# Kernel optimization log

Hardware: AMD Instinct MI355X
Metric: run time of the kernel (lower is better)

The kernel has to match this reference:

```python
import jax, jax.numpy as jnp
import numpy as np

B, S, D, H = 2, 2048, 1024, 16


def setup_inputs() -> dict:
    key = jax.random.key(0)
    kq, kk, kv1, kv2 = jax.random.split(key, 4)
    return {
        "q": jax.random.normal(kq, (B, S, D), dtype=jnp.float32),
        "k": jax.random.normal(kk, (B, S, D), dtype=jnp.float32),
        "v1": jax.random.normal(kv1, (B, S, D), dtype=jnp.float32),
        "v2": jax.random.normal(kv2, (B, S, D), dtype=jnp.float32),
        "num_attn_heads": 16,
    }


def _split_heads(x, h):
    b, s, d = x.shape
    return x.reshape(b, s, h, d // h).transpose(0, 2, 1, 3)  # [B,H,S,dh]


def reference(q, k, v1, v2, num_attn_heads):
    h = num_attn_heads
    b, s, d = q.shape
    dh = d // h
    qh = _split_heads(q, h)
    kh = _split_heads(k, h)
    v1h = _split_heads(v1, h)
    v2h = _split_heads(v2, h)
    scores = jnp.einsum("bhqd,bhkd->bhqk", qh, kh) / jnp.sqrt(jnp.float32(dh))
    # Faithful to create_mask(input, 0): nopeek = triu(ones, k=0); mask = (nopeek == 0)
    # -> only STRICTLY lower triangle is visible; diagonal and above get -1e9.
    # Row 0 is fully masked -> softmax uniform (same as torch behavior).
    allowed = jnp.tril(jnp.ones((s, s), dtype=bool), k=-1)  # [S,S] j < i
    scores = jnp.where(allowed[None, None], scores, jnp.float32(-1e9))
    p_attn = jax.nn.softmax(scores, axis=-1)  # dropout p=0.0 -> identity
    o1 = jnp.einsum("bhqk,bhkd->bhqd", p_attn, v1h)
    o2 = jnp.einsum("bhqk,bhkd->bhqd", p_attn, v2h)
    o1 = o1.transpose(0, 2, 1, 3).reshape(b, s, d)
    o2 = o2.transpose(0, 2, 1, 3).reshape(b, s, d)
    return (o1, o2)
```

## Files before the change

### kernel.cpp

```cpp
#include <hip/hip_runtime.h>

#define B_ 2
#define S_ 2048
#define D_ 1024
#define H_ 16
#define DH 64
#define OFF2 (B_ * S_ * D_)
#define ELEMS (B_ * H_ * S_ * DH)

typedef __attribute__((ext_vector_type(8))) __bf16 bf16x8;
typedef __attribute__((ext_vector_type(4))) float f32x4;
typedef __attribute__((ext_vector_type(4))) unsigned int u32x4;
typedef __attribute__((ext_vector_type(2))) unsigned int u32x2;
typedef __attribute__((address_space(3))) unsigned int lds_u32;
typedef __attribute__((address_space(1))) const unsigned int glob_u32;

__device__ __forceinline__ unsigned short f2bf(float f) {
    return __builtin_bit_cast(unsigned short, (__bf16)f);
}
__device__ __forceinline__ unsigned int pk2(float a, float b) {
    return (unsigned int)f2bf(a) | ((unsigned int)f2bf(b) << 16);
}
__device__ __forceinline__ float bf2f(unsigned short h) {
    unsigned int u = ((unsigned int)h) << 16;
    return __builtin_bit_cast(float, u);
}

__global__ void prep_all(const float* __restrict__ k,
                         const float* __restrict__ v1, const float* __restrict__ v2,
                         unsigned short* __restrict__ kb,
                         unsigned short* __restrict__ v1t, unsigned short* __restrict__ v2t) {
    int id = blockIdx.x;
    if (id < 2048) {
        int cid = id * 256 + threadIdx.x;
        int d8 = cid & 7;
        int s  = (cid >> 3) & (S_ - 1);
        int h  = (cid >> 14) & (H_ - 1);
        int b  = cid >> 18;
        int off = (b * S_ + s) * D_ + h * DH + d8 * 8;
        float4 f0 = *(const float4*)(k + off);
        float4 f1 = *(const float4*)(k + off + 4);
        u32x4 wv = {pk2(f0.x, f0.y), pk2(f0.z, f0.w),
                    pk2(f1.x, f1.y), pk2(f1.z, f1.w)};
        *(u32x4*)(kb + cid * 8) = wv;
        return;
    }
    __shared__ __align__(16) unsigned short ldsT[64][72];
    int id2 = id - 2048;
    int t = threadIdx.x;
    int s0 = (id2 & 31) * 64;
    int bh = (id2 >> 5) & 31;
    int b = bh >> 4, h = bh & 15;
    const float* src = (id2 >> 10) ? v2 : v1;
    unsigned short* dst = (id2 >> 10) ? v2t : v1t;
    {
        int sl = t >> 2, dc = t & 3;
        int off = (b * S_ + s0 + sl) * D_ + h * DH + dc * 16;
#pragma unroll
        for (int i4 = 0; i4 < 4; i4++) {
            float4 f = *(const float4*)(src + off + i4 * 4);
            int d = dc * 16 + i4 * 4;
            ldsT[d + 0][sl] = f2bf(f.x);
            ldsT[d + 1][sl] = f2bf(f.y);
            ldsT[d + 2][sl] = f2bf(f.z);
            ldsT[d + 3][sl] = f2bf(f.w);
        }
    }
    __syncthreads();
    {
        int d = t >> 2, sc = t & 3;
        u32x4 a = *(const u32x4*)(&ldsT[d][sc * 16]);
        u32x4 c = *(const u32x4*)(&ldsT[d][sc * 16 + 8]);
        int off = (bh * DH + d) * S_ + s0 + sc * 16;
        *(u32x4*)(dst + off) = a;
        *(u32x4*)(dst + off + 8) = c;
    }
}

__global__ __launch_bounds__(256) void flash_attn(
        const float* __restrict__ qf, const unsigned short* __restrict__ kb,
        const unsigned short* __restrict__ v1t, const unsigned short* __restrict__ v2t,
        float* __restrict__ out) {
    __shared__ __align__(16) unsigned short sK0[4096], sK1[4096];
    __shared__ __align__(16) unsigned short sV1[4096], sV2[4096];

    int tid = threadIdx.x;
    int w = tid >> 6, lane = tid & 63;
    int lr = lane & 15, lg = lane >> 4;
    int srow = tid >> 3, sco = tid & 7;

    int id = blockIdx.x;
    int xcd = id & 7;
    int j = id >> 3;
    int bh = xcd * 4 + (j & 3);
    int qt = 31 - (j >> 2);
    int b = bh >> 4, hh = bh & 15;

    const unsigned short* gK  = kb  + bh * (S_ * DH);
    const unsigned short* gV1 = v1t + bh * (DH * S_);
    const unsigned short* gV2 = v2t + bh * (DH * S_);

    auto stageV = [&](int t) {
#pragma unroll
        for (int jj = 0; jj < 2; jj++) {
            int row = srow + jj * 32;
            int cosw = (sco ^ (row & 7)) * 8;
            int c8 = (tid + jj * 256) * 8;
            __builtin_amdgcn_global_load_lds((glob_u32*)(gV1 + row * S_ + t * 64 + cosw),
                                             (lds_u32*)(sV1 + c8), 16, 0, 0);
            __builtin_amdgcn_global_load_lds((glob_u32*)(gV2 + row * S_ + t * 64 + cosw),
                                             (lds_u32*)(sV2 + c8), 16, 0, 0);
        }
    };
    auto stageK = [&](unsigned short* dK, int t) {
#pragma unroll
        for (int jj = 0; jj < 2; jj++) {
            int row = srow + jj * 32;
            int cosw = (sco ^ (row & 7)) * 8;
            int c8 = (tid + jj * 256) * 8;
            __builtin_amdgcn_global_load_lds((glob_u32*)(gK + (t * 64 + row) * 64 + cosw),
                                             (lds_u32*)(dK + c8), 16, 0, 0);
        }
    };

    bf16x8 qa[2];
    {
        const float qs = 0.125f * 1.4426950408889634f;
        const float* a = qf + ((size_t)b * S_ + qt * 64 + w * 16 + lr) * D_ + hh * DH + lg * 8;
        float4 q0 = *(const float4*)a;
        float4 q1 = *(const float4*)(a + 4);
        float4 q2 = *(const float4*)(a + 32);
        float4 q3 = *(const float4*)(a + 36);
        u32x4 w0 = {pk2(q0.x * qs, q0.y * qs), pk2(q0.z * qs, q0.w * qs),
                    pk2(q1.x * qs, q1.y * qs), pk2(q1.z * qs, q1.w * qs)};
        u32x4 w1 = {pk2(q2.x * qs, q2.y * qs), pk2(q2.z * qs, q2.w * qs),
                    pk2(q3.x * qs, q3.y * qs), pk2(q3.z * qs, q3.w * qs)};
        qa[0] = __builtin_bit_cast(bf16x8, w0);
        qa[1] = __builtin_bit_cast(bf16x8, w1);
    }

    f32x4 acc1[4], acc2[4];
#pragma unroll
    for (int dt = 0; dt < 4; dt++) {
        acc1[dt] = (f32x4){0.f, 0.f, 0.f, 0.f};
        acc2[dt] = (f32x4){0.f, 0.f, 0.f, 0.f};
    }
    float l = 0.f;

    stageK(sK0, 0);

    for (int t = 0; t <= qt; t++) {
        const unsigned short* cK = (t & 1) ? sK1 : sK0;
        unsigned short* nK       = (t & 1) ? sK0 : sK1;
        __builtin_amdgcn_s_barrier();
        stageV(t);
        stageK(nK, (t < qt) ? t + 1 : qt);
        asm volatile("s_waitcnt vmcnt(6)" ::: "memory");
        f32x4 s[4];
        __builtin_amdgcn_s_setprio(1);
#pragma unroll
        for (int n = 0; n < 4; n++) {
            int kv = n * 16 + lr;
            int ix0 = ((kv << 6) + lg * 8) ^ ((kv & 7) << 3);
            int ix1 = ((kv << 6) + 32 + lg * 8) ^ ((kv & 7) << 3);
            bf16x8 k0 = __builtin_bit_cast(bf16x8, *(const u32x4*)(cK + ix0));
            bf16x8 k1 = __builtin_bit_cast(bf16x8, *(const u32x4*)(cK + ix1));
            f32x4 a = __builtin_amdgcn_mfma_f32_16x16x32_bf16(
                k0, qa[0], (f32x4){-20.f, -20.f, -20.f, -20.f}, 0, 0, 0);
            s[n] = __builtin_amdgcn_mfma_f32_16x16x32_bf16(k1, qa[1], a, 0, 0, 0);
        }
        __builtin_amdgcn_s_setprio(0);
        if (t == qt) {
#pragma unroll
            for (int n = 0; n < 4; n++)
#pragma unroll
                for (int r = 0; r < 4; r++)
                    if (n * 16 + lg * 4 + r >= w * 16 + lr) s[n][r] = -1e30f;
        }
        u32x4 pa[2];
#pragma unroll
        for (int ks = 0; ks < 2; ks++) {
            float p0[4], p1[4];
#pragma unroll
            for (int r = 0; r < 4; r++) {
                p0[r] = __builtin_amdgcn_exp2f(s[2 * ks][r] - 20.0f);
                p1[r] = __builtin_amdgcn_exp2f(s[2 * ks + 1][r] - 20.0f);
                l += p0[r] + p1[r];
            }
            unsigned int u0 = pk2(p0[0], p0[1]);
            unsigned int u1 = pk2(p0[2], p0[3]);
            unsigned int u2 = pk2(p1[0], p1[1]);
            unsigned int u3 = pk2(p1[2], p1[3]);
            u32x2 ab = __builtin_amdgcn_permlane32_swap(u0, u2, false, false);
            u32x2 cd = __builtin_amdgcn_permlane32_swap(u1, u3, false, false);
            u32x2 ab2 = __builtin_amdgcn_permlane16_swap(ab[0], ab[1], false, false);
            u32x2 cd2 = __builtin_amdgcn_permlane16_swap(cd[0], cd[1], false, false);
            pa[ks] = (u32x4){ab2[0], cd2[0], ab2[1], cd2[1]};
        }
        asm volatile("s_waitcnt vmcnt(2)" ::: "memory");
        __builtin_amdgcn_s_barrier();
        __builtin_amdgcn_s_setprio(1);
#pragma unroll
        for (int ks = 0; ks < 2; ks++) {
            bf16x8 pab = __builtin_bit_cast(bf16x8, pa[ks]);
#pragma unroll
            for (int dt = 0; dt < 4; dt++) {
                int d = dt * 16 + lr;
                int vix = ((d << 6) + ks * 32 + lg * 8) ^ ((d & 7) << 3);
                bf16x8 vf1 = __builtin_bit_cast(bf16x8, *(const u32x4*)(sV1 + vix));
                acc1[dt] = __builtin_amdgcn_mfma_f32_16x16x32_bf16(vf1, pab, acc1[dt], 0, 0, 0);
                bf16x8 vf2 = __builtin_bit_cast(bf16x8, *(const u32x4*)(sV2 + vix));
                acc2[dt] = __builtin_amdgcn_mfma_f32_16x16x32_bf16(vf2, pab, acc2[dt], 0, 0, 0);
            }
        }
        __builtin_amdgcn_s_setprio(0);
    }

    asm volatile("s_waitcnt vmcnt(0)" ::: "memory");

    float lt = l;
    lt += __shfl_xor(lt, 16, 64);
    lt += __shfl_xor(lt, 32, 64);
    float inv = 1.0f / lt;
    {
        int qrow = qt * 64 + w * 16 + lr;
        int base = (b * S_ + qrow) * D_ + hh * DH + lg * 4;
#pragma unroll
        for (int dt = 0; dt < 4; dt++) {
            f32x4 o1 = acc1[dt] * inv;
            f32x4 o2 = acc2[dt] * inv;
            *(f32x4*)(out + base + dt * 16) = o1;
            *(f32x4*)(out + base + dt * 16 + OFF2) = o2;
        }
    }
}

__global__ void row0_mean(const unsigned short* __restrict__ v1t,
                          const unsigned short* __restrict__ v2t,
                          float* __restrict__ out) {
    int wid = blockIdx.x * 4 + (threadIdx.x >> 6);
    int lane = threadIdx.x & 63;
    int tz = wid >> 11;
    int bhd = wid & 2047;
    const unsigned short* src = (tz ? v2t : v1t) + bhd * S_;
    float sum = 0.f;
#pragma unroll
    for (int kk = 0; kk < 4; kk++) {
        u32x4 v = *(const u32x4*)(src + (kk * 64 + lane) * 8);
#pragma unroll
        for (int jj = 0; jj < 4; jj++) {
            unsigned int u = v[jj];
            sum += bf2f((unsigned short)(u & 0xffff)) + bf2f((unsigned short)(u >> 16));
        }
    }
#pragma unroll
    for (int msk = 32; msk >= 1; msk >>= 1) sum += __shfl_xor(sum, msk, 64);
    if (lane == 0) {
        int b = bhd >> 10, rem = bhd & 1023, h = rem >> 6, d = rem & 63;
        out[tz * OFF2 + b * (S_ * D_) + h * DH + d] = sum * (1.0f / S_);
    }
}

extern "C" void kernel_launch(void* const* d_in, const int* in_sizes, int n_in,
                              void* d_out, int out_size, void* d_ws, size_t ws_size,
                              hipStream_t stream) {
    const float* q  = (const float*)d_in[0];
    const float* k  = (const float*)d_in[1];
    const float* v1 = (const float*)d_in[2];
    const float* v2 = (const float*)d_in[3];
    float* out = (float*)d_out;

    unsigned short* kb  = (unsigned short*)d_ws;
    unsigned short* v1t = kb + ELEMS;
    unsigned short* v2t = v1t + ELEMS;

    prep_all<<<4096, 256, 0, stream>>>(k, v1, v2, kb, v1t, v2t);
    flash_attn<<<1024, 256, 0, stream>>>(q, kb, v1t, v2t, out);
    row0_mean<<<1024, 256, 0, stream>>>(v1t, v2t, out);
}
```

Baseline: 66.69 us.

## Fold row-0 mean into attention kernel and prefetch first K/V tiles early

Removes the separate row0_mean launch by appending 1024 extra blocks to flash_attn that compute the uniform-softmax output for row 0. Attention blocks now skip writing row 0 so the two block types do not write the same output. The prologue now issues the Q loads and the first K, V and next-K tile transfers before the Q bf16 conversion, so memory latency overlaps setup, and the loop skips the barrier and staging on its first iteration. The redundant -20 subtraction before exp2 is dropped, since the MFMA accumulator init already applies that offset and the normalisation cancels it.

```diff
diff --git a/kernel.cpp b/kernel.cpp
--- a/kernel.cpp
+++ b/kernel.cpp
@@ -85,11 +85,37 @@
     __shared__ __align__(16) unsigned short sV1[4096], sV2[4096];
 
     int tid = threadIdx.x;
+    int id = blockIdx.x;
+
+    if (id >= 1024) {
+        int wid = (id - 1024) * 4 + (tid >> 6);
+        int lane = tid & 63;
+        int tz = wid >> 11;
+        int bhd = wid & 2047;
+        const unsigned short* src = (tz ? v2t : v1t) + bhd * S_;
+        float sum = 0.f;
+#pragma unroll
+        for (int kk = 0; kk < 4; kk++) {
+            u32x4 v = *(const u32x4*)(src + (kk * 64 + lane) * 8);
+#pragma unroll
+            for (int jj = 0; jj < 4; jj++) {
+                unsigned int u = v[jj];
+                sum += bf2f((unsigned short)(u & 0xffff)) + bf2f((unsigned short)(u >> 16));
+            }
+        }
+#pragma unroll
+        for (int msk = 32; msk >= 1; msk >>= 1) sum += __shfl_xor(sum, msk, 64);
+        if (lane == 0) {
+            int b = bhd >> 10, rem = bhd & 1023, h = rem >> 6, d = rem & 63;
+            out[tz * OFF2 + b * (S_ * D_) + h * DH + d] = sum * (1.0f / S_);
+        }
+        return;
+    }
+
     int w = tid >> 6, lane = tid & 63;
     int lr = lane & 15, lg = lane >> 4;
     int srow = tid >> 3, sco = tid & 7;
 
-    int id = blockIdx.x;
     int xcd = id & 7;
     int j = id >> 3;
     int bh = xcd * 4 + (j & 3);
@@ -123,14 +149,19 @@
         }
     };
 
+    const float* qsrc = qf + ((size_t)b * S_ + qt * 64 + w * 16 + lr) * D_ + hh * DH + lg * 8;
+    float4 q0 = *(const float4*)qsrc;
+    float4 q1 = *(const float4*)(qsrc + 4);
+    float4 q2 = *(const float4*)(qsrc + 32);
+    float4 q3 = *(const float4*)(qsrc + 36);
+
+    stageK(sK0, 0);
+    stageV(0);
+    stageK(sK1, (qt >= 1) ? 1 : 0);
+
     bf16x8 qa[2];
     {
         const float qs = 0.125f * 1.4426950408889634f;
-        const float* a = qf + ((size_t)b * S_ + qt * 64 + w * 16 + lr) * D_ + hh * DH + lg * 8;
-        float4 q0 = *(const float4*)a;
-        float4 q1 = *(const float4*)(a + 4);
-        float4 q2 = *(const float4*)(a + 32);
-        float4 q3 = *(const float4*)(a + 36);
         u32x4 w0 = {pk2(q0.x * qs, q0.y * qs), pk2(q0.z * qs, q0.w * qs),
                     pk2(q1.x * qs, q1.y * qs), pk2(q1.z * qs, q1.w * qs)};
         u32x4 w1 = {pk2(q2.x * qs, q2.y * qs), pk2(q2.z * qs, q2.w * qs),
@@ -147,14 +178,14 @@
     }
     float l = 0.f;
 
-    stageK(sK0, 0);
-
     for (int t = 0; t <= qt; t++) {
         const unsigned short* cK = (t & 1) ? sK1 : sK0;
         unsigned short* nK       = (t & 1) ? sK0 : sK1;
-        __builtin_amdgcn_s_barrier();
-        stageV(t);
-        stageK(nK, (t < qt) ? t + 1 : qt);
+        if (t > 0) {
+            __builtin_amdgcn_s_barrier();
+            stageV(t);
+            stageK(nK, (t < qt) ? t + 1 : qt);
+        }
         asm volatile("s_waitcnt vmcnt(6)" ::: "memory");
         f32x4 s[4];
         __builtin_amdgcn_s_setprio(1);
@@ -183,8 +214,8 @@
             float p0[4], p1[4];
 #pragma unroll
             for (int r = 0; r < 4; r++) {
-                p0[r] = __builtin_amdgcn_exp2f(s[2 * ks][r] - 20.0f);
-                p1[r] = __builtin_amdgcn_exp2f(s[2 * ks + 1][r] - 20.0f);
+                p0[r] = __builtin_amdgcn_exp2f(s[2 * ks][r]);
+                p1[r] = __builtin_amdgcn_exp2f(s[2 * ks + 1][r]);
                 l += p0[r] + p1[r];
             }
             unsigned int u0 = pk2(p0[0], p0[1]);
@@ -224,40 +255,16 @@
     float inv = 1.0f / lt;
     {
         int qrow = qt * 64 + w * 16 + lr;
-        int base = (b * S_ + qrow) * D_ + hh * DH + lg * 4;
-#pragma unroll
-        for (int dt = 0; dt < 4; dt++) {
-            f32x4 o1 = acc1[dt] * inv;
-            f32x4 o2 = acc2[dt] * inv;
-            *(f32x4*)(out + base + dt * 16) = o1;
-            *(f32x4*)(out + base + dt * 16 + OFF2) = o2;
-        }
-    }
-}
-
-__global__ void row0_mean(const unsigned short* __restrict__ v1t,
-                          const unsigned short* __restrict__ v2t,
-                          float* __restrict__ out) {
-    int wid = blockIdx.x * 4 + (threadIdx.x >> 6);
-    int lane = threadIdx.x & 63;
-    int tz = wid >> 11;
-    int bhd = wid & 2047;
-    const unsigned short* src = (tz ? v2t : v1t) + bhd * S_;
-    float sum = 0.f;
-#pragma unroll
-    for (int kk = 0; kk < 4; kk++) {
-        u32x4 v = *(const u32x4*)(src + (kk * 64 + lane) * 8);
-#pragma unroll
-        for (int jj = 0; jj < 4; jj++) {
-            unsigned int u = v[jj];
-            sum += bf2f((unsigned short)(u & 0xffff)) + bf2f((unsigned short)(u >> 16));
-        }
-    }
-#pragma unroll
-    for (int msk = 32; msk >= 1; msk >>= 1) sum += __shfl_xor(sum, msk, 64);
-    if (lane == 0) {
-        int b = bhd >> 10, rem = bhd & 1023, h = rem >> 6, d = rem & 63;
-        out[tz * OFF2 + b * (S_ * D_) + h * DH + d] = sum * (1.0f / S_);
+        if (qrow != 0) {
+            int base = (b * S_ + qrow) * D_ + hh * DH + lg * 4;
+#pragma unroll
+            for (int dt = 0; dt < 4; dt++) {
+                f32x4 o1 = acc1[dt] * inv;
+                f32x4 o2 = acc2[dt] * inv;
+                *(f32x4*)(out + base + dt * 16) = o1;
+                *(f32x4*)(out + base + dt * 16 + OFF2) = o2;
+            }
+        }
     }
 }
 
@@ -275,6 +282,5 @@
     unsigned short* v2t = v1t + ELEMS;
 
     prep_all<<<4096, 256, 0, stream>>>(k, v1, v2, kb, v1t, v2t);
-    flash_attn<<<1024, 256, 0, stream>>>(q, kb, v1t, v2t, out);
-    row0_mean<<<1024, 256, 0, stream>>>(v1t, v2t, out);
-}
+    flash_attn<<<2048, 256, 0, stream>>>(q, kb, v1t, v2t, out);
+}
```

Result: faster. 61.95 us (median of 2 runs) (-7.1%).
